# Optimization experiments

Measured on AMD Instinct MI355X. Metric: run time of the kernel, lower is better.

## Reference

```python
import jax, jax.numpy as jnp
import numpy as np

TEMPLATE_SUBDIVISION = 8
SIGMA = 0.5
NORMALISED = True


def setup_inputs() -> dict:
    key = jax.random.key(0)
    k1, k2, k3 = jax.random.split(key, 3)
    B, N, M_full, D = 2, 32768, 8192, 3
    x = jax.random.normal(k1, (B, N, D), dtype=jnp.float32)
    deformed_verts = jax.random.normal(k2, (B, M_full, D), dtype=jnp.float32)
    mean_shape_verts = jax.random.normal(k3, (B, M_full, D), dtype=jnp.float32)
    deformation_parameters = jnp.zeros((1,), dtype=jnp.float32)  # unused by transform
    return {
        "x": x,
        "deformed_verts": deformed_verts,
        "mean_shape_verts": mean_shape_verts,
        "deformation_parameters": deformation_parameters,
    }


def reference(x, deformed_verts, mean_shape_verts, deformation_parameters):
    # subsample template vertices: [B, M_full, D] -> [B, M, D]
    dv = deformed_verts[:, ::TEMPLATE_SUBDIVISION]
    mv = mean_shape_verts[:, ::TEMPLATE_SUBDIVISION]
    inv_sigma2 = 1.0 / (SIGMA ** 2)
    # broadcast RBF-like kernel: [B, M, N, D]
    kernel_res = jnp.exp(-jnp.abs(x[:, None, :, :] - dv[:, :, None, :]) * inv_sigma2)
    # weighted sum over control vertices M -> [B, N, D]
    out = jnp.sum(mv[:, :, None, :] * kernel_res, axis=1)
    if NORMALISED:
        denominator = jnp.sum(kernel_res, axis=1)
        out = out / denominator
    return out
```

## Files before the change

kernel.cpp:

```cpp
#include <hip/hip_runtime.h>
#include <math.h>

constexpr int B       = 2;
constexpr int N       = 32768;
constexpr int D       = 3;
constexpr int M_FULL  = 8192;
constexpr int SUBDIV  = 8;
constexpr int M       = M_FULL / SUBDIV;
constexpr int K       = 512;
constexpr float LO    = -4.0f;
constexpr float INV_W = 64.0f;
constexpr float K4    = 5.770780163555852f;

constexpr int BLOCK   = 256;
constexpr int CHUNKS  = N / BLOCK;
constexpr int GRID    = B * D * CHUNKS;
constexpr int VPT     = M / BLOCK;

__device__ inline void scan512_pre(float* a) {
    const int lane = threadIdx.x & 63;
    const int base = lane * 8;
    float xv[8], e[8]; float ls = 0.f;
    #pragma unroll
    for (int t = 0; t < 8; ++t) xv[t] = a[base + t];
    #pragma unroll
    for (int t = 0; t < 8; ++t) { e[t] = ls; ls += xv[t]; }
    float inc = ls;
    #pragma unroll
    for (int off = 1; off < 64; off <<= 1) {
        const float tmp = __shfl_up(inc, off, 64);
        if (lane >= off) inc += tmp;
    }
    const float exoff = inc - ls;
    #pragma unroll
    for (int t = 0; t < 8; ++t) a[base + t] = exoff + e[t];
}

__device__ inline void scan512_suf(float* a) {
    const int lane = threadIdx.x & 63;
    const int base = lane * 8;
    float xv[8], e[8]; float ls = 0.f;
    #pragma unroll
    for (int t = 0; t < 8; ++t) xv[t] = a[base + t];
    #pragma unroll
    for (int t = 7; t >= 0; --t) { e[t] = ls; ls += xv[t]; }
    float inc = ls;
    #pragma unroll
    for (int off = 1; off < 64; off <<= 1) {
        const float tmp = __shfl_down(inc, off, 64);
        if (lane + off < 64) inc += tmp;
    }
    const float exoff = inc - ls;
    #pragma unroll
    for (int t = 0; t < 8; ++t) a[base + t] = exoff + e[t] + xv[t];
}

__device__ inline void scan512_i(const int* cntA, int* begA, int* curA) {
    const int lane = threadIdx.x & 63;
    const int base = lane * 8;
    int xv[8], e[8]; int ls = 0;
    #pragma unroll
    for (int t = 0; t < 8; ++t) xv[t] = cntA[base + t];
    #pragma unroll
    for (int t = 0; t < 8; ++t) { e[t] = ls; ls += xv[t]; }
    int inc = ls;
    #pragma unroll
    for (int off = 1; off < 64; off <<= 1) {
        const int tmp = __shfl_up(inc, off, 64);
        if (lane >= off) inc += tmp;
    }
    const int exoff = inc - ls;
    #pragma unroll
    for (int t = 0; t < 8; ++t) {
        begA[base + t] = exoff + e[t];
        curA[base + t] = exoff + e[t];
    }
}

__global__ __launch_bounds__(BLOCK) void deformer_fused(
    const float* __restrict__ x,
    const float* __restrict__ dverts,
    const float* __restrict__ mverts,
    float* __restrict__ out)
{
    __shared__ float2 vw[M];
    __shared__ float  gAp[K], gSp[K], gAm[K], gSm[K];
    __shared__ int    cnt[K], beg[K], cur[K];

    const int tid = threadIdx.x;
    const int p = blockIdx.x >> 7;
    const int c = blockIdx.x & 127;
    const int b = p / 3, d = p % 3;

    const int n = c * BLOCK + tid;
    const int o = (b * N + n) * D + d;
    const float xq = x[o];

    cnt[tid] = 0;       cnt[tid + 256] = 0;
    gAp[tid] = 0.f;     gAp[tid + 256] = 0.f;
    gSp[tid] = 0.f;     gSp[tid + 256] = 0.f;
    gAm[tid] = 0.f;     gAm[tid + 256] = 0.f;
    gSm[tid] = 0.f;     gSm[tid + 256] = 0.f;
    __syncthreads();

    float vv[VPT], wv[VPT];
    #pragma unroll
    for (int r = 0; r < VPT; ++r) {
        const int m = tid + r * BLOCK;
        const int g = (b * M_FULL + m * SUBDIV) * D + d;
        vv[r] = dverts[g];
        wv[r] = mverts[g];
    }
    int bjv[VPT];
    #pragma unroll
    for (int r = 0; r < VPT; ++r) {
        const float v = vv[r], w = wv[r];
        const float epv = __builtin_amdgcn_exp2f( K4 * v);
        const float emv = __builtin_amdgcn_exp2f(-K4 * v);
        int bj = (int)floorf((v - LO) * INV_W);
        bj = bj < 0 ? 0 : (bj > K - 1 ? K - 1 : bj);
        bjv[r] = bj;
        atomicAdd(&cnt[bj], 1);
        atomicAdd(&gAp[bj], w * epv);
        atomicAdd(&gSp[bj], epv);
        atomicAdd(&gAm[bj], w * emv);
        atomicAdd(&gSm[bj], emv);
    }
    __syncthreads();

    const int wid = tid >> 6;
    if      (wid == 0) { scan512_i(cnt, beg, cur); scan512_suf(gSm); }
    else if (wid == 1) scan512_pre(gAp);
    else if (wid == 2) scan512_pre(gSp);
    else if (wid == 3) scan512_suf(gAm);
    __syncthreads();

    #pragma unroll
    for (int r = 0; r < VPT; ++r) {
        const int pos = atomicAdd(&cur[bjv[r]], 1);
        vw[pos] = make_float2(vv[r], wv[r]);
    }
    __syncthreads();

    int j = (int)floorf((xq - LO) * INV_W);
    j = j < 0 ? 0 : (j > K - 1 ? K - 1 : j);

    const float en  = __builtin_amdgcn_exp2f(-K4 * xq);
    const float epx = __builtin_amdgcn_exp2f( K4 * xq);

    const float Ap = gAp[j], Sp = gSp[j];
    const float Am = (j < K - 1) ? gAm[j + 1] : 0.f;
    const float Sm = (j < K - 1) ? gSm[j + 1] : 0.f;

    const int s0 = beg[j], s1 = cur[j];
    float rN = 0.f, rD = 0.f;
    for (int i = s0; i < s1; ++i) {
        const float2 pv = vw[i];
        const float e2 = __builtin_amdgcn_exp2f(-K4 * fabsf(xq - pv.x));
        rN += pv.y * e2;
        rD += e2;
    }
    out[o] = (en * Ap + epx * Am + rN) / (en * Sp + epx * Sm + rD);
}

extern "C" void kernel_launch(void* const* d_in, const int* in_sizes, int n_in,
                              void* d_out, int out_size, void* d_ws, size_t ws_size,
                              hipStream_t stream) {
    const float* x  = (const float*)d_in[0];
    const float* dv = (const float*)d_in[1];
    const float* mv = (const float*)d_in[2];
    float* out = (float*)d_out;

    deformer_fused<<<GRID, BLOCK, 0, stream>>>(x, dv, mv, out);
}
```

Baseline: 78.63 us.

## Use 1024-thread blocks and replace float shared atomics with per-bin reductions

Raises the block size to 1024 so each thread loads exactly one control vertex, and each block amortises the per-block histogram and scan setup over four times as many query points, with a quarter as many blocks. The float atomic accumulation of the four per-bin sums is replaced by a counting-sort pass followed by a per-bin sequential reduction over the sorted vertices, leaving only an integer atomic histogram. This adds an extra synchronisation phase and uneven per-bin loop lengths. It also cuts the grid to 192 blocks, which may leave parts of the GPU idle.

```diff
diff --git a/kernel.cpp b/kernel.cpp
--- a/kernel.cpp
+++ b/kernel.cpp
@@ -12,10 +12,9 @@
 constexpr float INV_W = 64.0f;
 constexpr float K4    = 5.770780163555852f;
 
-constexpr int BLOCK   = 256;
+constexpr int BLOCK   = 1024;
 constexpr int CHUNKS  = N / BLOCK;
 constexpr int GRID    = B * D * CHUNKS;
-constexpr int VPT     = M / BLOCK;
 
 __device__ inline void scan512_pre(float* a) {
     const int lane = threadIdx.x & 63;
@@ -88,58 +87,52 @@
     __shared__ int    cnt[K], beg[K], cur[K];
 
     const int tid = threadIdx.x;
-    const int p = blockIdx.x >> 7;
-    const int c = blockIdx.x & 127;
+    const int p = blockIdx.x >> 5;
+    const int c = blockIdx.x & 31;
     const int b = p / 3, d = p % 3;
 
     const int n = c * BLOCK + tid;
     const int o = (b * N + n) * D + d;
     const float xq = x[o];
 
-    cnt[tid] = 0;       cnt[tid + 256] = 0;
-    gAp[tid] = 0.f;     gAp[tid + 256] = 0.f;
-    gSp[tid] = 0.f;     gSp[tid + 256] = 0.f;
-    gAm[tid] = 0.f;     gAm[tid + 256] = 0.f;
-    gSm[tid] = 0.f;     gSm[tid + 256] = 0.f;
+    const int g = (b * M_FULL + tid * SUBDIV) * D + d;
+    const float v = dverts[g];
+    const float w = mverts[g];
+
+    if (tid < K) cnt[tid] = 0;
     __syncthreads();
 
-    float vv[VPT], wv[VPT];
-    #pragma unroll
-    for (int r = 0; r < VPT; ++r) {
-        const int m = tid + r * BLOCK;
-        const int g = (b * M_FULL + m * SUBDIV) * D + d;
-        vv[r] = dverts[g];
-        wv[r] = mverts[g];
-    }
-    int bjv[VPT];
-    #pragma unroll
-    for (int r = 0; r < VPT; ++r) {
-        const float v = vv[r], w = wv[r];
-        const float epv = __builtin_amdgcn_exp2f( K4 * v);
-        const float emv = __builtin_amdgcn_exp2f(-K4 * v);
-        int bj = (int)floorf((v - LO) * INV_W);
-        bj = bj < 0 ? 0 : (bj > K - 1 ? K - 1 : bj);
-        bjv[r] = bj;
-        atomicAdd(&cnt[bj], 1);
-        atomicAdd(&gAp[bj], w * epv);
-        atomicAdd(&gSp[bj], epv);
-        atomicAdd(&gAm[bj], w * emv);
-        atomicAdd(&gSm[bj], emv);
+    int bj = (int)floorf((v - LO) * INV_W);
+    bj = bj < 0 ? 0 : (bj > K - 1 ? K - 1 : bj);
+    atomicAdd(&cnt[bj], 1);
+    __syncthreads();
+
+    if (tid < 64) scan512_i(cnt, beg, cur);
+    __syncthreads();
+
+    const int pos = atomicAdd(&cur[bj], 1);
+    vw[pos] = make_float2(v, w);
+    __syncthreads();
+
+    if (tid < K) {
+        const int s0 = beg[tid], s1 = cur[tid];
+        float ap = 0.f, sp = 0.f, am = 0.f, sm = 0.f;
+        for (int i = s0; i < s1; ++i) {
+            const float2 pv = vw[i];
+            const float epv = __builtin_amdgcn_exp2f( K4 * pv.x);
+            const float emv = __builtin_amdgcn_exp2f(-K4 * pv.x);
+            ap += pv.y * epv; sp += epv;
+            am += pv.y * emv; sm += emv;
+        }
+        gAp[tid] = ap; gSp[tid] = sp; gAm[tid] = am; gSm[tid] = sm;
     }
     __syncthreads();
 
     const int wid = tid >> 6;
-    if      (wid == 0) { scan512_i(cnt, beg, cur); scan512_suf(gSm); }
-    else if (wid == 1) scan512_pre(gAp);
-    else if (wid == 2) scan512_pre(gSp);
-    else if (wid == 3) scan512_suf(gAm);
-    __syncthreads();
-
-    #pragma unroll
-    for (int r = 0; r < VPT; ++r) {
-        const int pos = atomicAdd(&cur[bjv[r]], 1);
-        vw[pos] = make_float2(vv[r], wv[r]);
-    }
+    if      (wid == 0) scan512_pre(gAp);
+    else if (wid == 1) scan512_pre(gSp);
+    else if (wid == 2) scan512_suf(gAm);
+    else if (wid == 3) scan512_suf(gSm);
     __syncthreads();
 
     int j = (int)floorf((xq - LO) * INV_W);
```

Result: faster. 63.98 us (-18.6%).
